# Kernel optimization log

Measured on AMD Instinct MI355X. Metric: run time of the kernel, lower is better.

Reference implementation:

```python
import jax, jax.numpy as jnp
import numpy as np
from jax import lax

B, P, ENC, DEC, ATT, EMB, V, L = 64, 196, 2048, 512, 512, 512, 10000, 30


def setup_inputs() -> dict:
    key = jax.random.key(0)
    ks = jax.random.split(key, 24)
    s = 0.02
    encoder_out = jax.random.normal(ks[0], (B, P, ENC), dtype=jnp.float32)
    encoded_captions = jax.random.randint(ks[1], (B, L), 0, V, dtype=jnp.int64)
    caption_lengths = jax.random.randint(ks[2], (B, 1), 2, L + 1, dtype=jnp.int64)
    # ensure max decode length == L-1 (matches torch max(decode_lengths))
    caption_lengths = caption_lengths.at[0, 0].set(L)
    p = lambda k, sh: jax.random.normal(k, sh, dtype=jnp.float32) * s
    return {
        "encoder_out": encoder_out,
        "encoded_captions": encoded_captions,
        "caption_lengths": caption_lengths,
        "W_enc": p(ks[3], (ATT, ENC)), "b_enc": jnp.zeros((ATT,), jnp.float32),
        "W_dec": p(ks[4], (ATT, DEC)), "b_dec": jnp.zeros((ATT,), jnp.float32),
        "w_full": p(ks[5], (ATT,)), "b_full": jnp.zeros((), jnp.float32),
        "emb_table": jax.random.uniform(ks[6], (V, EMB), jnp.float32, -0.1, 0.1),
        "W_ih": p(ks[7], (4 * DEC, EMB + ENC)), "b_ih": jnp.zeros((4 * DEC,), jnp.float32),
        "W_hh": p(ks[8], (4 * DEC, DEC)), "b_hh": jnp.zeros((4 * DEC,), jnp.float32),
        "W_init_h": p(ks[9], (DEC, ENC)), "b_init_h": jnp.zeros((DEC,), jnp.float32),
        "W_init_c": p(ks[10], (DEC, ENC)), "b_init_c": jnp.zeros((DEC,), jnp.float32),
        "W_beta": p(ks[11], (ENC, DEC)), "b_beta": jnp.zeros((ENC,), jnp.float32),
        "W_fc": jax.random.uniform(ks[12], (V, DEC), jnp.float32, -0.1, 0.1),
        "b_fc": jnp.zeros((V,), jnp.float32),
    }


def reference(encoder_out, encoded_captions, caption_lengths,
              W_enc, b_enc, W_dec, b_dec, w_full, b_full, emb_table,
              W_ih, b_ih, W_hh, b_hh, W_init_h, b_init_h, W_init_c, b_init_c,
              W_beta, b_beta, W_fc, b_fc):
    lengths = caption_lengths[:, 0]
    sort_ind = jnp.argsort(-lengths)  # descending, stable
    enc = encoder_out[sort_ind]            # [B,P,ENC]
    caps = encoded_captions[sort_ind]      # [B,L]
    dec_lens = lengths[sort_ind] - 1       # [B]
    T = caps.shape[1] - 1

    embs = emb_table[caps]                 # [B,L,EMB]
    mean_enc = enc.mean(axis=1)
    h0 = mean_enc @ W_init_h.T + b_init_h
    c0 = mean_enc @ W_init_c.T + b_init_c
    # encoder attention projection is h-independent: compute once
    att1 = jnp.einsum('bpe,ae->bpa', enc, W_enc) + b_enc  # [B,P,ATT]

    def step(carry, xs):
        h, c = carry
        emb_t, mask_t = xs  # [B,EMB], [B] bool
        att2 = h @ W_dec.T + b_dec                              # [B,ATT]
        e = jax.nn.relu(att1 + att2[:, None, :]) @ w_full + b_full  # [B,P]
        alpha = jax.nn.softmax(e, axis=1)
        awe = jnp.einsum('bp,bpe->be', alpha, enc)              # [B,ENC]
        gate = jax.nn.sigmoid(h @ W_beta.T + b_beta)
        awe = gate * awe
        x = jnp.concatenate([emb_t, awe], axis=1)               # [B,EMB+ENC]
        gates = x @ W_ih.T + b_ih + h @ W_hh.T + b_hh           # [B,4D]
        i, f, g, o = jnp.split(gates, 4, axis=1)
        i, f, o = jax.nn.sigmoid(i), jax.nn.sigmoid(f), jax.nn.sigmoid(o)
        g = jnp.tanh(g)
        c_new = f * c + i * g
        h_new = o * jnp.tanh(c_new)
        preds = h_new @ W_fc.T + b_fc                           # [B,V]  (dropout: eval/identity)
        m = mask_t[:, None].astype(preds.dtype)
        return (h_new, c_new), (preds * m, alpha * m)

    mask = jnp.arange(T)[:, None] < dec_lens[None, :]           # [T,B]
    embs_t = jnp.swapaxes(embs[:, :T], 0, 1)                    # [T,B,EMB]
    _, (preds, alphas) = lax.scan(step, (h0, c0), (embs_t, mask))
    predictions = jnp.swapaxes(preds, 0, 1)                     # [B,T,V]
    alphas = jnp.swapaxes(alphas, 0, 1)                         # [B,T,P]
    return predictions, alphas, caps, dec_lens, sort_ind
```

## Files before the change

### kernel.cpp

```cpp
#include <hip/hip_runtime.h>
#include <hip/hip_bf16.h>
#include <math.h>
#include <float.h>

#define BDIM   64
#define PDIM   196
#define ENC    2048
#define DECD   512
#define ATTD   512
#define EMBD   512
#define VOC    10000
#define LCAP   30
#define TSTEPS 29

typedef __attribute__((ext_vector_type(8))) short s8v;
typedef __attribute__((ext_vector_type(4))) float f4v;

__device__ __forceinline__ float sigf(float x) { return 1.0f / (1.0f + expf(-x)); }
__device__ __forceinline__ float bf2f(ushort u) { return __uint_as_float(((uint)u) << 16); }

__global__ void sort_kernel(const int* __restrict__ cap_len,
                            const int* __restrict__ caps,
                            int* __restrict__ sort_ind,
                            int* __restrict__ dec_lens,
                            int* __restrict__ caps_s,
                            float* __restrict__ out_caps,
                            float* __restrict__ out_dlen,
                            float* __restrict__ out_sind) {
    int i = threadIdx.x;
    __shared__ int len[BDIM];
    len[i] = cap_len[i];
    __syncthreads();
    int li = len[i];
    int r = 0;
    for (int j = 0; j < BDIM; ++j) {
        int lj = len[j];
        if (lj > li || (lj == li && j < i)) ++r;
    }
    sort_ind[r] = i;
    dec_lens[r] = li - 1;
    out_sind[r] = (float)i;
    out_dlen[r] = (float)(li - 1);
    for (int tt = 0; tt < LCAP; ++tt) {
        int v = caps[i * LCAP + tt];
        caps_s[r * LCAP + tt] = v;
        out_caps[r * LCAP + tt] = (float)v;
    }
}

__global__ __launch_bounds__(256) void conv_enc_kernel(const float* __restrict__ enc,
                                                       const int* __restrict__ sort_ind,
                                                       __hip_bfloat16* __restrict__ enc_s,
                                                       float* __restrict__ mean_enc) {
    int b = blockIdx.y, tid = threadIdx.x;
    int e = (blockIdx.x << 8) + tid;
    const float* ep = enc + (size_t)sort_ind[b] * (PDIM * ENC) + e;
    __hip_bfloat16* op = enc_s + (size_t)b * (PDIM * ENC) + e;
    float s = 0.f;
    for (int p = 0; p < PDIM; ++p) {
        float v = ep[(size_t)p * ENC];
        s += v;
        op[(size_t)p * ENC] = __float2bfloat16(v);
    }
    mean_enc[(size_t)b * ENC + e] = s * (1.0f / (float)PDIM);
}

__global__ __launch_bounds__(256) void f2b_kernel(const float* __restrict__ src,
                                                  __hip_bfloat16* __restrict__ dst, int n) {
    int i = blockIdx.x * 256 + threadIdx.x;
    if (i < n) dst[i] = __float2bfloat16(src[i]);
}

__global__ __launch_bounds__(256) void h0_kernel(const float* __restrict__ h0f,
                                                 __hip_bfloat16* __restrict__ xh) {
    int idx = blockIdx.x * 256 + threadIdx.x;
    int b = idx >> 9, j = idx & 511;
    xh[(size_t)b * 3072 + 2560 + j] = __float2bfloat16(h0f[idx]);
}

__global__ __launch_bounds__(256) void gemm32_k(
    const float* __restrict__ A, int lda,
    const float* __restrict__ W0, const float* __restrict__ bias0,
    float* __restrict__ C, int ldc, int K) {
    __shared__ float As[16][64];
    __shared__ float Ws[16][64];
    const int tid = threadIdx.x;
    const int tx = tid & 15, ty = tid >> 4;
    const int bn0 = blockIdx.x * 64;
    const int lr = tid >> 2;
    const int lk = (tid & 3) << 2;
    const float* Arow = A + (size_t)lr * lda;
    const int wn = bn0 + lr;
    float acc[4][4];
#pragma unroll
    for (int i = 0; i < 4; ++i)
#pragma unroll
        for (int j = 0; j < 4; ++j) acc[i][j] = 0.f;
    for (int k0 = 0; k0 < K; k0 += 16) {
        float4 av = *(const float4*)(Arow + k0 + lk);
        float4 wv = *(const float4*)(W0 + (size_t)wn * K + k0 + lk);
        __syncthreads();
        As[lk + 0][lr] = av.x; As[lk + 1][lr] = av.y;
        As[lk + 2][lr] = av.z; As[lk + 3][lr] = av.w;
        Ws[lk + 0][lr] = wv.x; Ws[lk + 1][lr] = wv.y;
        Ws[lk + 2][lr] = wv.z; Ws[lk + 3][lr] = wv.w;
        __syncthreads();
#pragma unroll
        for (int kk = 0; kk < 16; ++kk) {
            const float4 a = *(const float4*)&As[kk][ty << 2];
            const float4 w = *(const float4*)&Ws[kk][tx << 2];
            acc[0][0] += a.x * w.x; acc[0][1] += a.x * w.y; acc[0][2] += a.x * w.z; acc[0][3] += a.x * w.w;
            acc[1][0] += a.y * w.x; acc[1][1] += a.y * w.y; acc[1][2] += a.y * w.z; acc[1][3] += a.y * w.w;
            acc[2][0] += a.z * w.x; acc[2][1] += a.z * w.y; acc[2][2] += a.z * w.z; acc[2][3] += a.z * w.w;
            acc[3][0] += a.w * w.x; acc[3][1] += a.w * w.y; acc[3][2] += a.w * w.z; acc[3][3] += a.w * w.w;
        }
    }
#pragma unroll
    for (int i = 0; i < 4; ++i) {
        int row = (ty << 2) + i;
#pragma unroll
        for (int j = 0; j < 4; ++j) {
            int col = bn0 + (tx << 2) + j;
            C[(size_t)row * ldc + col] = acc[i][j] + bias0[col];
        }
    }
}

enum { E_ATT1 = 0, E_GACT = 1, E_GATES = 2, E_PREDS = 3 };

template <int MF, int MODE, int KA, int KB, bool XM>
__global__ __launch_bounds__(64) void mfma_gemm(
    const __hip_bfloat16* __restrict__ A, int lda,
    const __hip_bfloat16* __restrict__ W0, const __hip_bfloat16* __restrict__ W1,
    const float* __restrict__ bias0, const float* __restrict__ bias1,
    void* __restrict__ Cv,
    const int* __restrict__ dec_lens, int t) {
    const int l = threadIdx.x;
    const int c16 = l & 15, kg = l >> 4;
    const int n0 = (XM ? (int)blockIdx.y : (int)blockIdx.x) * 64;
    const int m0 = (XM ? (int)blockIdx.x : (int)blockIdx.y) * (16 * MF);

    f4v acc[MF][4];
#pragma unroll
    for (int mi = 0; mi < MF; ++mi)
#pragma unroll
        for (int ni = 0; ni < 4; ++ni) acc[mi][ni] = (f4v)0.0f;

    const __hip_bfloat16* arow[MF];
#pragma unroll
    for (int mi = 0; mi < MF; ++mi)
        arow[mi] = A + (size_t)(m0 + mi * 16 + c16) * lda + kg * 8;

    const __hip_bfloat16* w0r[4];
    const __hip_bfloat16* w1r[4];
#pragma unroll
    for (int ni = 0; ni < 4; ++ni) {
        int n = n0 + ni * 16 + c16;
        if (MODE == E_GACT) {
            w0r[ni] = (n < 2048) ? W0 + (size_t)n * 512 : W1 + (size_t)(n - 2048) * 512;
        } else if (MODE == E_GATES) {
            w0r[ni] = W0 + (size_t)n * (KA);
            w1r[ni] = W1 + (size_t)n * (KB);
        } else if (MODE == E_PREDS) {
            int nn = (n < VOC) ? n : (VOC - 1);
            w0r[ni] = W0 + (size_t)nn * KA;
        } else {
            w0r[ni] = W0 + (size_t)n * KA;
        }
        w0r[ni] += kg * 8;
        if (MODE == E_GATES) w1r[ni] += kg * 8;
    }

#pragma unroll 8
    for (int k0 = 0; k0 < KA; k0 += 32) {
        s8v a[MF], b[4];
#pragma unroll
        for (int mi = 0; mi < MF; ++mi) a[mi] = *(const s8v*)(arow[mi] + k0);
#pragma unroll
        for (int ni = 0; ni < 4; ++ni) b[ni] = *(const s8v*)(w0r[ni] + k0);
#pragma unroll
        for (int mi = 0; mi < MF; ++mi)
#pragma unroll
            for (int ni = 0; ni < 4; ++ni)
                acc[mi][ni] = __builtin_amdgcn_mfma_f32_16x16x32_bf16(a[mi], b[ni], acc[mi][ni], 0, 0, 0);
    }
    if constexpr (KB > 0) {
#pragma unroll
        for (int k0 = 0; k0 < KB; k0 += 32) {
            s8v a[MF], b[4];
#pragma unroll
            for (int mi = 0; mi < MF; ++mi) a[mi] = *(const s8v*)(arow[mi] + KA + k0);
#pragma unroll
            for (int ni = 0; ni < 4; ++ni) b[ni] = *(const s8v*)(w1r[ni] + k0);
#pragma unroll
            for (int mi = 0; mi < MF; ++mi)
#pragma unroll
                for (int ni = 0; ni < 4; ++ni)
                    acc[mi][ni] = __builtin_amdgcn_mfma_f32_16x16x32_bf16(a[mi], b[ni], acc[mi][ni], 0, 0, 0);
        }
    }

#pragma unroll
    for (int mi = 0; mi < MF; ++mi) {
#pragma unroll
        for (int ni = 0; ni < 4; ++ni) {
#pragma unroll
            for (int i = 0; i < 4; ++i) {
                int r = m0 + mi * 16 + kg * 4 + i;
                int c = n0 + ni * 16 + c16;
                float v = acc[mi][ni][i];
                if (MODE == E_ATT1) {
                    ((__hip_bfloat16*)Cv)[(size_t)r * 512 + c] = __float2bfloat16(v + bias0[c]);
                } else if (MODE == E_GACT) {
                    float* C = (float*)Cv;
                    if (c < 2048) C[(size_t)r * 2560 + c] = sigf(v + bias0[c]);
                    else          C[(size_t)r * 2560 + c] = v + bias1[c - 2048];
                } else if (MODE == E_GATES) {
                    ((float*)Cv)[(size_t)r * 2048 + c] = v + bias0[c] + bias1[c];
                } else {
                    if (c < VOC) {
                        float o = v + bias0[c];
                        ((float*)Cv)[(size_t)r * (TSTEPS * VOC) + (size_t)t * VOC + c] =
                            (t < dec_lens[r]) ? o : 0.f;
                    }
                }
            }
        }
    }
}

__global__ __launch_bounds__(256) void attawe_kernel(
    const __hip_bfloat16* __restrict__ att1, const float* __restrict__ gact,
    const __hip_bfloat16* __restrict__ enc_s,
    const float* __restrict__ w_full, const float* __restrict__ b_full,
    const float* __restrict__ emb_table,
    const int* __restrict__ caps_s, const int* __restrict__ dec_lens,
    __hip_bfloat16* __restrict__ xh, float* __restrict__ out_alphas, int t) {
    int b = blockIdx.x;
    int tid = threadIdx.x;
    __shared__ float s_att2[ATTD];
    __shared__ float s_wf[ATTD];
    __shared__ float s_e[PDIM];
    __shared__ float red[256];

    s_att2[tid]       = gact[(size_t)b * 2560 + 2048 + tid];
    s_att2[tid + 256] = gact[(size_t)b * 2560 + 2048 + 256 + tid];
    s_wf[tid]       = w_full[tid];
    s_wf[tid + 256] = w_full[tid + 256];
    __syncthreads();

    int wv = tid >> 6, lane = tid & 63;
    const float bf = b_full[0];
    const int a0 = lane << 3;
    for (int p = wv; p < PDIM; p += 4) {
        const ushort* row = (const ushort*)att1 + ((size_t)b * PDIM + p) * ATTD + a0;
        float s = 0.f;
#pragma unroll
        for (int i = 0; i < 8; ++i) {
            float x = bf2f(row[i]) + s_att2[a0 + i];
            s += fmaxf(x, 0.f) * s_wf[a0 + i];
        }
#pragma unroll
        for (int off = 32; off; off >>= 1) s += __shfl_xor(s, off);
        if (lane == 0) s_e[p] = s + bf;
    }
    __syncthreads();

    float v = (tid < PDIM) ? s_e[tid] : -FLT_MAX;
    red[tid] = v;
    __syncthreads();
    for (int st = 128; st; st >>= 1) {
        if (tid < st) red[tid] = fmaxf(red[tid], red[tid + st]);
        __syncthreads();
    }
    float mx = red[0];
    __syncthreads();
    float ex = (tid < PDIM) ? expf(v - mx) : 0.f;
    red[tid] = ex;
    __syncthreads();
    for (int st = 128; st; st >>= 1) {
        if (tid < st) red[tid] += red[tid + st];
        __syncthreads();
    }
    float inv = 1.f / red[0];
    __syncthreads();
    if (tid < PDIM) {
        float al = ex * inv;
        s_e[tid] = al;
        out_alphas[(size_t)b * (TSTEPS * PDIM) + (size_t)t * PDIM + tid] =
            (t < dec_lens[b]) ? al : 0.f;
    }
    __syncthreads();

    int e = tid << 3;
    const ushort* ep = (const ushort*)enc_s + (size_t)b * (PDIM * ENC) + e;
    float acc[8];
#pragma unroll
    for (int i = 0; i < 8; ++i) acc[i] = 0.f;
#pragma unroll 2
    for (int p = 0; p < PDIM; ++p) {
        float al = s_e[p];
        s8v u = *(const s8v*)(ep + (size_t)p * ENC);
#pragma unroll
        for (int i = 0; i < 8; ++i) acc[i] += al * bf2f((ushort)u[i]);
    }
    float4 g0 = *(const float4*)(gact + (size_t)b * 2560 + e);
    float4 g1 = *(const float4*)(gact + (size_t)b * 2560 + e + 4);
    __hip_bfloat16 ob[8];
    ob[0] = __float2bfloat16(acc[0] * g0.x); ob[1] = __float2bfloat16(acc[1] * g0.y);
    ob[2] = __float2bfloat16(acc[2] * g0.z); ob[3] = __float2bfloat16(acc[3] * g0.w);
    ob[4] = __float2bfloat16(acc[4] * g1.x); ob[5] = __float2bfloat16(acc[5] * g1.y);
    ob[6] = __float2bfloat16(acc[6] * g1.z); ob[7] = __float2bfloat16(acc[7] * g1.w);
    *(uint4*)(xh + (size_t)b * 3072 + 512 + e) = *(uint4*)ob;

    if (tid < 128) {
        int cap = caps_s[b * LCAP + t];
        int j = tid << 2;
        float4 em = *(const float4*)(emb_table + (size_t)cap * EMBD + j);
        __hip_bfloat16 eb[4];
        eb[0] = __float2bfloat16(em.x); eb[1] = __float2bfloat16(em.y);
        eb[2] = __float2bfloat16(em.z); eb[3] = __float2bfloat16(em.w);
        *(uint2*)(xh + (size_t)b * 3072 + j) = *(uint2*)eb;
    }
}

__global__ __launch_bounds__(256) void cell_kernel(const float* __restrict__ gates,
                                                   float* __restrict__ c,
                                                   __hip_bfloat16* __restrict__ xh) {
    int idx = blockIdx.x * 256 + threadIdx.x;
    int b = idx >> 9, j = idx & 511;
    const float* g = gates + (size_t)b * 2048;
    float i_ = sigf(g[j]);
    float f_ = sigf(g[512 + j]);
    float g_ = tanhf(g[1024 + j]);
    float o_ = sigf(g[1536 + j]);
    float cn = f_ * c[idx] + i_ * g_;
    c[idx] = cn;
    xh[(size_t)b * 3072 + 2560 + j] = __float2bfloat16(o_ * tanhf(cn));
}

extern "C" void kernel_launch(void* const* d_in, const int* in_sizes, int n_in,
                              void* d_out, int out_size, void* d_ws, size_t ws_size,
                              hipStream_t stream) {
    const float* enc      = (const float*)d_in[0];
    const int*   caps     = (const int*)d_in[1];
    const int*   clen     = (const int*)d_in[2];
    const float* W_enc    = (const float*)d_in[3];
    const float* b_enc    = (const float*)d_in[4];
    const float* W_dec    = (const float*)d_in[5];
    const float* b_dec    = (const float*)d_in[6];
    const float* w_full   = (const float*)d_in[7];
    const float* b_full   = (const float*)d_in[8];
    const float* emb_tab  = (const float*)d_in[9];
    const float* W_ih     = (const float*)d_in[10];
    const float* b_ih     = (const float*)d_in[11];
    const float* W_hh     = (const float*)d_in[12];
    const float* b_hh     = (const float*)d_in[13];
    const float* W_init_h = (const float*)d_in[14];
    const float* b_init_h = (const float*)d_in[15];
    const float* W_init_c = (const float*)d_in[16];
    const float* b_init_c = (const float*)d_in[17];
    const float* W_beta   = (const float*)d_in[18];
    const float* b_beta   = (const float*)d_in[19];
    const float* W_fc     = (const float*)d_in[20];
    const float* b_fc     = (const float*)d_in[21];

    float* out_pred = (float*)d_out;
    float* out_alph = out_pred + (size_t)BDIM * TSTEPS * VOC;
    float* out_caps = out_alph + (size_t)BDIM * TSTEPS * PDIM;
    float* out_dlen = out_caps + BDIM * LCAP;
    float* out_sind = out_dlen + BDIM;

    char* p = (char*)d_ws;
    auto carve = [&](size_t bytes) { char* r = p; p += (bytes + 255) & ~(size_t)255; return r; };
    int* sort_ind = (int*)carve(64 * 4);
    int* dec_lens = (int*)carve(64 * 4);
    int* caps_s   = (int*)carve(64 * LCAP * 4);
    float* mean_e = (float*)carve((size_t)64 * ENC * 4);
    float* h0f    = (float*)carve((size_t)64 * 512 * 4);
    float* cbuf   = (float*)carve((size_t)64 * 512 * 4);
    float* gact   = (float*)carve((size_t)64 * 2560 * 4);
    float* gates  = (float*)carve((size_t)64 * 2048 * 4);
    __hip_bfloat16* xh     = (__hip_bfloat16*)carve((size_t)64 * 3072 * 2);
    __hip_bfloat16* enc_s  = (__hip_bfloat16*)carve((size_t)64 * PDIM * ENC * 2);
    __hip_bfloat16* att1   = (__hip_bfloat16*)carve((size_t)64 * PDIM * 512 * 2);
    __hip_bfloat16* Wb_enc = (__hip_bfloat16*)carve((size_t)512 * 2048 * 2);
    __hip_bfloat16* Wb_bet = (__hip_bfloat16*)carve((size_t)2048 * 512 * 2);
    __hip_bfloat16* Wb_dec = (__hip_bfloat16*)carve((size_t)512 * 512 * 2);
    __hip_bfloat16* Wb_ih  = (__hip_bfloat16*)carve((size_t)2048 * 2560 * 2);
    __hip_bfloat16* Wb_hh  = (__hip_bfloat16*)carve((size_t)2048 * 512 * 2);
    __hip_bfloat16* Wb_fc  = (__hip_bfloat16*)carve((size_t)VOC * 512 * 2);

    sort_kernel<<<1, 64, 0, stream>>>(clen, caps, sort_ind, dec_lens, caps_s,
                                      out_caps, out_dlen, out_sind);
    conv_enc_kernel<<<dim3(8, 64), 256, 0, stream>>>(enc, sort_ind, enc_s, mean_e);
    f2b_kernel<<<(512 * 2048 + 255) / 256, 256, 0, stream>>>(W_enc, Wb_enc, 512 * 2048);
    f2b_kernel<<<(2048 * 512 + 255) / 256, 256, 0, stream>>>(W_beta, Wb_bet, 2048 * 512);
    f2b_kernel<<<(512 * 512 + 255) / 256, 256, 0, stream>>>(W_dec, Wb_dec, 512 * 512);
    f2b_kernel<<<(2048 * 2560 + 255) / 256, 256, 0, stream>>>(W_ih, Wb_ih, 2048 * 2560);
    f2b_kernel<<<(2048 * 512 + 255) / 256, 256, 0, stream>>>(W_hh, Wb_hh, 2048 * 512);
    f2b_kernel<<<(VOC * 512 + 255) / 256, 256, 0, stream>>>(W_fc, Wb_fc, VOC * 512);

    gemm32_k<<<dim3(8, 1), 256, 0, stream>>>(mean_e, ENC, W_init_h, b_init_h, h0f, 512, ENC);
    gemm32_k<<<dim3(8, 1), 256, 0, stream>>>(mean_e, ENC, W_init_c, b_init_c, cbuf, 512, ENC);
    h0_kernel<<<128, 256, 0, stream>>>(h0f, xh);

    mfma_gemm<2, E_ATT1, 2048, 0, true><<<dim3(392, 8), 64, 0, stream>>>(
        enc_s, ENC, Wb_enc, nullptr, b_enc, nullptr, att1, nullptr, 0);

    for (int t = 0; t < TSTEPS; ++t) {
        mfma_gemm<1, E_GACT, 512, 0, false><<<dim3(40, 4), 64, 0, stream>>>(
            xh + 2560, 3072, Wb_bet, Wb_dec, b_beta, b_dec, gact, nullptr, 0);
        attawe_kernel<<<64, 256, 0, stream>>>(att1, gact, enc_s, w_full, b_full,
                                              emb_tab, caps_s, dec_lens, xh,
                                              out_alph, t);
        mfma_gemm<1, E_GATES, 2560, 512, false><<<dim3(32, 4), 64, 0, stream>>>(
            xh, 3072, Wb_ih, Wb_hh, b_ih, b_hh, gates, nullptr, 0);
        cell_kernel<<<128, 256, 0, stream>>>(gates, cbuf, xh);
        mfma_gemm<1, E_PREDS, 512, 0, false><<<dim3(160, 4), 64, 0, stream>>>(
            xh + 2560, 3072, Wb_fc, nullptr, b_fc, nullptr, out_pred, dec_lens, t);
    }
}
```

Measured before the change: 3.655 ms.

## Batch vocab projection after loop, split-K recurrent GEMMs, prefetch MFMA operands

The per-step vocabulary projection is taken out of the recurrence. Each step's hidden state is stored, and a single large GEMM over all 29×64 rows runs after the loop. The gate and attention-projection GEMMs are split along K into two partial buffers so more workgroups run in each step, and bias, sigmoid and sum are folded into the attawe and cell kernels. A three-slot register prefetch pipeline is added to the shared MFMA inner loop. This costs extra partial-sum traffic and an hstore buffer in exchange for shorter serial steps and better weight reuse in the FC projection.

```diff
diff --git a/kernel.cpp b/kernel.cpp
--- a/kernel.cpp
+++ b/kernel.cpp
@@ -18,6 +18,31 @@
 
 __device__ __forceinline__ float sigf(float x) { return 1.0f / (1.0f + expf(-x)); }
 __device__ __forceinline__ float bf2f(ushort u) { return __uint_as_float(((uint)u) << 16); }
+
+template <int MF, int NIT>
+__device__ __forceinline__ void gemm_seg(const __hip_bfloat16* const* arow,
+                                         const __hip_bfloat16* const* wrow,
+                                         f4v acc[][4]) {
+    s8v aP[3][MF], bP[3][4];
+    auto LD = [&](int it, int slot) {
+#pragma unroll
+        for (int mi = 0; mi < MF; ++mi) aP[slot][mi] = *(const s8v*)(arow[mi] + it * 32);
+#pragma unroll
+        for (int ni = 0; ni < 4; ++ni)  bP[slot][ni] = *(const s8v*)(wrow[ni] + it * 32);
+    };
+    LD(0, 0);
+    if constexpr (NIT > 1) LD(1, 1);
+#pragma unroll
+    for (int it = 0; it < NIT; ++it) {
+        if (it + 2 < NIT) LD(it + 2, (it + 2) % 3);
+        const int s = it % 3;
+#pragma unroll
+        for (int mi = 0; mi < MF; ++mi)
+#pragma unroll
+            for (int ni = 0; ni < 4; ++ni)
+                acc[mi][ni] = __builtin_amdgcn_mfma_f32_16x16x32_bf16(aP[s][mi], bP[s][ni], acc[mi][ni], 0, 0, 0);
+    }
+}
 
 __global__ void sort_kernel(const int* __restrict__ cap_len,
                             const int* __restrict__ caps,
@@ -126,116 +151,159 @@
     }
 }
 
-enum { E_ATT1 = 0, E_GACT = 1, E_GATES = 2, E_PREDS = 3 };
-
-template <int MF, int MODE, int KA, int KB, bool XM>
-__global__ __launch_bounds__(64) void mfma_gemm(
-    const __hip_bfloat16* __restrict__ A, int lda,
-    const __hip_bfloat16* __restrict__ W0, const __hip_bfloat16* __restrict__ W1,
-    const float* __restrict__ bias0, const float* __restrict__ bias1,
-    void* __restrict__ Cv,
-    const int* __restrict__ dec_lens, int t) {
-    const int l = threadIdx.x;
-    const int c16 = l & 15, kg = l >> 4;
-    const int n0 = (XM ? (int)blockIdx.y : (int)blockIdx.x) * 64;
-    const int m0 = (XM ? (int)blockIdx.x : (int)blockIdx.y) * (16 * MF);
-
-    f4v acc[MF][4];
-#pragma unroll
-    for (int mi = 0; mi < MF; ++mi)
+__global__ __launch_bounds__(64) void att1_gemm(
+    const __hip_bfloat16* __restrict__ A, const __hip_bfloat16* __restrict__ W,
+    const float* __restrict__ bias, __hip_bfloat16* __restrict__ C) {
+    const int l = threadIdx.x, c16 = l & 15, kg = l >> 4;
+    const int m0 = blockIdx.x * 32, n0 = blockIdx.y * 64;
+    f4v acc[2][4];
+#pragma unroll
+    for (int mi = 0; mi < 2; ++mi)
 #pragma unroll
         for (int ni = 0; ni < 4; ++ni) acc[mi][ni] = (f4v)0.0f;
-
-    const __hip_bfloat16* arow[MF];
-#pragma unroll
-    for (int mi = 0; mi < MF; ++mi)
-        arow[mi] = A + (size_t)(m0 + mi * 16 + c16) * lda + kg * 8;
-
-    const __hip_bfloat16* w0r[4];
-    const __hip_bfloat16* w1r[4];
-#pragma unroll
-    for (int ni = 0; ni < 4; ++ni) {
-        int n = n0 + ni * 16 + c16;
-        if (MODE == E_GACT) {
-            w0r[ni] = (n < 2048) ? W0 + (size_t)n * 512 : W1 + (size_t)(n - 2048) * 512;
-        } else if (MODE == E_GATES) {
-            w0r[ni] = W0 + (size_t)n * (KA);
-            w1r[ni] = W1 + (size_t)n * (KB);
-        } else if (MODE == E_PREDS) {
-            int nn = (n < VOC) ? n : (VOC - 1);
-            w0r[ni] = W0 + (size_t)nn * KA;
-        } else {
-            w0r[ni] = W0 + (size_t)n * KA;
-        }
-        w0r[ni] += kg * 8;
-        if (MODE == E_GATES) w1r[ni] += kg * 8;
-    }
-
-#pragma unroll 8
-    for (int k0 = 0; k0 < KA; k0 += 32) {
-        s8v a[MF], b[4];
-#pragma unroll
-        for (int mi = 0; mi < MF; ++mi) a[mi] = *(const s8v*)(arow[mi] + k0);
-#pragma unroll
-        for (int ni = 0; ni < 4; ++ni) b[ni] = *(const s8v*)(w0r[ni] + k0);
-#pragma unroll
-        for (int mi = 0; mi < MF; ++mi)
-#pragma unroll
-            for (int ni = 0; ni < 4; ++ni)
-                acc[mi][ni] = __builtin_amdgcn_mfma_f32_16x16x32_bf16(a[mi], b[ni], acc[mi][ni], 0, 0, 0);
-    }
-    if constexpr (KB > 0) {
-#pragma unroll
-        for (int k0 = 0; k0 < KB; k0 += 32) {
-            s8v a[MF], b[4];
-#pragma unroll
-            for (int mi = 0; mi < MF; ++mi) a[mi] = *(const s8v*)(arow[mi] + KA + k0);
-#pragma unroll
-            for (int ni = 0; ni < 4; ++ni) b[ni] = *(const s8v*)(w1r[ni] + k0);
-#pragma unroll
-            for (int mi = 0; mi < MF; ++mi)
-#pragma unroll
-                for (int ni = 0; ni < 4; ++ni)
-                    acc[mi][ni] = __builtin_amdgcn_mfma_f32_16x16x32_bf16(a[mi], b[ni], acc[mi][ni], 0, 0, 0);
-        }
-    }
-
-#pragma unroll
-    for (int mi = 0; mi < MF; ++mi) {
-#pragma unroll
-        for (int ni = 0; ni < 4; ++ni) {
+    const __hip_bfloat16* arow[2];
+#pragma unroll
+    for (int mi = 0; mi < 2; ++mi)
+        arow[mi] = A + (size_t)(m0 + mi * 16 + c16) * ENC + kg * 8;
+    const __hip_bfloat16* wrow[4];
+#pragma unroll
+    for (int ni = 0; ni < 4; ++ni)
+        wrow[ni] = W + (size_t)(n0 + ni * 16 + c16) * ENC + kg * 8;
+    gemm_seg<2, 64>(arow, wrow, acc);
+#pragma unroll
+    for (int mi = 0; mi < 2; ++mi)
+#pragma unroll
+        for (int ni = 0; ni < 4; ++ni)
 #pragma unroll
             for (int i = 0; i < 4; ++i) {
                 int r = m0 + mi * 16 + kg * 4 + i;
                 int c = n0 + ni * 16 + c16;
-                float v = acc[mi][ni][i];
-                if (MODE == E_ATT1) {
-                    ((__hip_bfloat16*)Cv)[(size_t)r * 512 + c] = __float2bfloat16(v + bias0[c]);
-                } else if (MODE == E_GACT) {
-                    float* C = (float*)Cv;
-                    if (c < 2048) C[(size_t)r * 2560 + c] = sigf(v + bias0[c]);
-                    else          C[(size_t)r * 2560 + c] = v + bias1[c - 2048];
-                } else if (MODE == E_GATES) {
-                    ((float*)Cv)[(size_t)r * 2048 + c] = v + bias0[c] + bias1[c];
-                } else {
-                    if (c < VOC) {
-                        float o = v + bias0[c];
-                        ((float*)Cv)[(size_t)r * (TSTEPS * VOC) + (size_t)t * VOC + c] =
-                            (t < dec_lens[r]) ? o : 0.f;
-                    }
+                C[(size_t)r * 512 + c] = __float2bfloat16(acc[mi][ni][i] + bias[c]);
+            }
+}
+
+__global__ __launch_bounds__(64) void gact_gemm(
+    const __hip_bfloat16* __restrict__ H,
+    const __hip_bfloat16* __restrict__ Wb,
+    const __hip_bfloat16* __restrict__ Wd,
+    float* __restrict__ P) {
+    const int l = threadIdx.x, c16 = l & 15, kg = l >> 4;
+    const int n0 = blockIdx.x * 64, m0 = blockIdx.y * 16, z = blockIdx.z;
+    const int ko = z * 256;
+    f4v acc[1][4];
+#pragma unroll
+    for (int ni = 0; ni < 4; ++ni) acc[0][ni] = (f4v)0.0f;
+    const __hip_bfloat16* arow[1] = { H + (size_t)(m0 + c16) * 3072 + ko + kg * 8 };
+    const __hip_bfloat16* wrow[4];
+#pragma unroll
+    for (int ni = 0; ni < 4; ++ni) {
+        int n = n0 + ni * 16 + c16;
+        wrow[ni] = ((n < 2048) ? Wb + (size_t)n * 512 : Wd + (size_t)(n - 2048) * 512) + ko + kg * 8;
+    }
+    gemm_seg<1, 8>(arow, wrow, acc);
+    float* Pz = P + (size_t)z * (64 * 2560);
+#pragma unroll
+    for (int ni = 0; ni < 4; ++ni)
+#pragma unroll
+        for (int i = 0; i < 4; ++i) {
+            int r = m0 + kg * 4 + i;
+            int c = n0 + ni * 16 + c16;
+            Pz[(size_t)r * 2560 + c] = acc[0][ni][i];
+        }
+}
+
+__global__ __launch_bounds__(64) void gates_gemm(
+    const __hip_bfloat16* __restrict__ X,
+    const __hip_bfloat16* __restrict__ Wih,
+    const __hip_bfloat16* __restrict__ Whh,
+    float* __restrict__ P) {
+    const int l = threadIdx.x, c16 = l & 15, kg = l >> 4;
+    const int n0 = blockIdx.x * 64, m0 = blockIdx.y * 16, z = blockIdx.z;
+    f4v acc[1][4];
+#pragma unroll
+    for (int ni = 0; ni < 4; ++ni) acc[0][ni] = (f4v)0.0f;
+    const __hip_bfloat16* arow[1];
+    const __hip_bfloat16* wrow[4];
+    if (z == 0) {
+        arow[0] = X + (size_t)(m0 + c16) * 3072 + kg * 8;
+#pragma unroll
+        for (int ni = 0; ni < 4; ++ni)
+            wrow[ni] = Wih + (size_t)(n0 + ni * 16 + c16) * 2560 + kg * 8;
+        gemm_seg<1, 48>(arow, wrow, acc);
+    } else {
+        arow[0] = X + (size_t)(m0 + c16) * 3072 + 1536 + kg * 8;
+#pragma unroll
+        for (int ni = 0; ni < 4; ++ni)
+            wrow[ni] = Wih + (size_t)(n0 + ni * 16 + c16) * 2560 + 1536 + kg * 8;
+        gemm_seg<1, 32>(arow, wrow, acc);
+        arow[0] = X + (size_t)(m0 + c16) * 3072 + 2560 + kg * 8;
+#pragma unroll
+        for (int ni = 0; ni < 4; ++ni)
+            wrow[ni] = Whh + (size_t)(n0 + ni * 16 + c16) * 512 + kg * 8;
+        gemm_seg<1, 16>(arow, wrow, acc);
+    }
+    float* Pz = P + (size_t)z * (64 * 2048);
+#pragma unroll
+    for (int ni = 0; ni < 4; ++ni)
+#pragma unroll
+        for (int i = 0; i < 4; ++i) {
+            int r = m0 + kg * 4 + i;
+            int c = n0 + ni * 16 + c16;
+            Pz[(size_t)r * 2048 + c] = acc[0][ni][i];
+        }
+}
+
+__global__ __launch_bounds__(64) void predsb_gemm(
+    const __hip_bfloat16* __restrict__ Hs,
+    const __hip_bfloat16* __restrict__ Wfc,
+    const float* __restrict__ bias,
+    const int* __restrict__ dec_lens,
+    float* __restrict__ out) {
+    const int l = threadIdx.x, c16 = l & 15, kg = l >> 4;
+    const int n0 = blockIdx.x * 64, m0 = blockIdx.y * 32;
+    f4v acc[2][4];
+#pragma unroll
+    for (int mi = 0; mi < 2; ++mi)
+#pragma unroll
+        for (int ni = 0; ni < 4; ++ni) acc[mi][ni] = (f4v)0.0f;
+    const __hip_bfloat16* arow[2];
+#pragma unroll
+    for (int mi = 0; mi < 2; ++mi)
+        arow[mi] = Hs + (size_t)(m0 + mi * 16 + c16) * 512 + kg * 8;
+    const __hip_bfloat16* wrow[4];
+#pragma unroll
+    for (int ni = 0; ni < 4; ++ni) {
+        int n = n0 + ni * 16 + c16;
+        int nn = (n < VOC) ? n : (VOC - 1);
+        wrow[ni] = Wfc + (size_t)nn * 512 + kg * 8;
+    }
+    gemm_seg<2, 16>(arow, wrow, acc);
+#pragma unroll
+    for (int mi = 0; mi < 2; ++mi)
+#pragma unroll
+        for (int ni = 0; ni < 4; ++ni)
+#pragma unroll
+            for (int i = 0; i < 4; ++i) {
+                int r = m0 + mi * 16 + kg * 4 + i;
+                int c = n0 + ni * 16 + c16;
+                if (c < VOC) {
+                    int tt = r >> 6, b = r & 63;
+                    float v = acc[mi][ni][i] + bias[c];
+                    out[(size_t)b * (TSTEPS * VOC) + (size_t)tt * VOC + c] =
+                        (tt < dec_lens[b]) ? v : 0.f;
                 }
             }
-        }
-    }
 }
 
 __global__ __launch_bounds__(256) void attawe_kernel(
-    const __hip_bfloat16* __restrict__ att1, const float* __restrict__ gact,
+    const __hip_bfloat16* __restrict__ att1, const float* __restrict__ gactp,
     const __hip_bfloat16* __restrict__ enc_s,
     const float* __restrict__ w_full, const float* __restrict__ b_full,
+    const float* __restrict__ b_dec, const float* __restrict__ b_beta,
     const float* __restrict__ emb_table,
     const int* __restrict__ caps_s, const int* __restrict__ dec_lens,
     __hip_bfloat16* __restrict__ xh, float* __restrict__ out_alphas, int t) {
+    const int G = 64 * 2560;
     int b = blockIdx.x;
     int tid = threadIdx.x;
     __shared__ float s_att2[ATTD];
@@ -243,8 +311,9 @@
     __shared__ float s_e[PDIM];
     __shared__ float red[256];
 
-    s_att2[tid]       = gact[(size_t)b * 2560 + 2048 + tid];
-    s_att2[tid + 256] = gact[(size_t)b * 2560 + 2048 + 256 + tid];
+    const float* gb = gactp + (size_t)b * 2560;
+    s_att2[tid]       = gb[2048 + tid]       + gb[G + 2048 + tid]       + b_dec[tid];
+    s_att2[tid + 256] = gb[2048 + 256 + tid] + gb[G + 2048 + 256 + tid] + b_dec[256 + tid];
     s_wf[tid]       = w_full[tid];
     s_wf[tid + 256] = w_full[tid + 256];
     __syncthreads();
@@ -304,13 +373,20 @@
 #pragma unroll
         for (int i = 0; i < 8; ++i) acc[i] += al * bf2f((ushort)u[i]);
     }
-    float4 g0 = *(const float4*)(gact + (size_t)b * 2560 + e);
-    float4 g1 = *(const float4*)(gact + (size_t)b * 2560 + e + 4);
+    float4 p00 = *(const float4*)(gb + e);
+    float4 p01 = *(const float4*)(gb + e + 4);
+    float4 p10 = *(const float4*)(gb + G + e);
+    float4 p11 = *(const float4*)(gb + G + e + 4);
+    float4 bb0 = *(const float4*)(b_beta + e);
+    float4 bb1 = *(const float4*)(b_beta + e + 4);
+    float g[8];
+    g[0] = sigf(p00.x + p10.x + bb0.x); g[1] = sigf(p00.y + p10.y + bb0.y);
+    g[2] = sigf(p00.z + p10.z + bb0.z); g[3] = sigf(p00.w + p10.w + bb0.w);
+    g[4] = sigf(p01.x + p11.x + bb1.x); g[5] = sigf(p01.y + p11.y + bb1.y);
+    g[6] = sigf(p01.z + p11.z + bb1.z); g[7] = sigf(p01.w + p11.w + bb1.w);
     __hip_bfloat16 ob[8];
-    ob[0] = __float2bfloat16(acc[0] * g0.x); ob[1] = __float2bfloat16(acc[1] * g0.y);
-    ob[2] = __float2bfloat16(acc[2] * g0.z); ob[3] = __float2bfloat16(acc[3] * g0.w);
-    ob[4] = __float2bfloat16(acc[4] * g1.x); ob[5] = __float2bfloat16(acc[5] * g1.y);
-    ob[6] = __float2bfloat16(acc[6] * g1.z); ob[7] = __float2bfloat16(acc[7] * g1.w);
+#pragma unroll
+    for (int i = 0; i < 8; ++i) ob[i] = __float2bfloat16(acc[i] * g[i]);
     *(uint4*)(xh + (size_t)b * 3072 + 512 + e) = *(uint4*)ob;
 
     if (tid < 128) {
@@ -324,19 +400,25 @@
     }
 }
 
-__global__ __launch_bounds__(256) void cell_kernel(const float* __restrict__ gates,
-                                                   float* __restrict__ c,
-                                                   __hip_bfloat16* __restrict__ xh) {
+__global__ __launch_bounds__(256) void cell_kernel(
+    const float* __restrict__ gatesp, const float* __restrict__ b_ih,
+    const float* __restrict__ b_hh, float* __restrict__ c,
+    __hip_bfloat16* __restrict__ xh, __hip_bfloat16* __restrict__ hstore, int t) {
+    const int GS = 64 * 2048;
     int idx = blockIdx.x * 256 + threadIdx.x;
     int b = idx >> 9, j = idx & 511;
-    const float* g = gates + (size_t)b * 2048;
-    float i_ = sigf(g[j]);
-    float f_ = sigf(g[512 + j]);
-    float g_ = tanhf(g[1024 + j]);
-    float o_ = sigf(g[1536 + j]);
-    float cn = f_ * c[idx] + i_ * g_;
+    const float* g0 = gatesp + (size_t)b * 2048;
+    const float* g1 = gatesp + GS + (size_t)b * 2048;
+    float vi = g0[j]        + g1[j]        + b_ih[j]        + b_hh[j];
+    float vf = g0[512 + j]  + g1[512 + j]  + b_ih[512 + j]  + b_hh[512 + j];
+    float vg = g0[1024 + j] + g1[1024 + j] + b_ih[1024 + j] + b_hh[1024 + j];
+    float vo = g0[1536 + j] + g1[1536 + j] + b_ih[1536 + j] + b_hh[1536 + j];
+    float i_ = sigf(vi), f_ = sigf(vf), gg = tanhf(vg), o_ = sigf(vo);
+    float cn = f_ * c[idx] + i_ * gg;
     c[idx] = cn;
-    xh[(size_t)b * 3072 + 2560 + j] = __float2bfloat16(o_ * tanhf(cn));
+    __hip_bfloat16 hb = __float2bfloat16(o_ * tanhf(cn));
+    xh[(size_t)b * 3072 + 2560 + j] = hb;
+    hstore[(size_t)t * (64 * 512) + idx] = hb;
 }
 
 extern "C" void kernel_launch(void* const* d_in, const int* in_sizes, int n_in,
@@ -379,9 +461,10 @@
     float* mean_e = (float*)carve((size_t)64 * ENC * 4);
     float* h0f    = (float*)carve((size_t)64 * 512 * 4);
     float* cbuf   = (float*)carve((size_t)64 * 512 * 4);
-    float* gact   = (float*)carve((size_t)64 * 2560 * 4);
-    float* gates  = (float*)carve((size_t)64 * 2048 * 4);
+    float* gactp  = (float*)carve((size_t)2 * 64 * 2560 * 4);
+    float* gatesp = (float*)carve((size_t)2 * 64 * 2048 * 4);
     __hip_bfloat16* xh     = (__hip_bfloat16*)carve((size_t)64 * 3072 * 2);
+    __hip_bfloat16* hstore = (__hip_bfloat16*)carve((size_t)TSTEPS * 64 * 512 * 2);
     __hip_bfloat16* enc_s  = (__hip_bfloat16*)carve((size_t)64 * PDIM * ENC * 2);
     __hip_bfloat16* att1   = (__hip_bfloat16*)carve((size_t)64 * PDIM * 512 * 2);
     __hip_bfloat16* Wb_enc = (__hip_bfloat16*)carve((size_t)512 * 2048 * 2);
@@ -405,19 +488,16 @@
     gemm32_k<<<dim3(8, 1), 256, 0, stream>>>(mean_e, ENC, W_init_c, b_init_c, cbuf, 512, ENC);
     h0_kernel<<<128, 256, 0, stream>>>(h0f, xh);
 
-    mfma_gemm<2, E_ATT1, 2048, 0, true><<<dim3(392, 8), 64, 0, stream>>>(
-        enc_s, ENC, Wb_enc, nullptr, b_enc, nullptr, att1, nullptr, 0);
+    att1_gemm<<<dim3(392, 8), 64, 0, stream>>>(enc_s, Wb_enc, b_enc, att1);
 
     for (int t = 0; t < TSTEPS; ++t) {
-        mfma_gemm<1, E_GACT, 512, 0, false><<<dim3(40, 4), 64, 0, stream>>>(
-            xh + 2560, 3072, Wb_bet, Wb_dec, b_beta, b_dec, gact, nullptr, 0);
-        attawe_kernel<<<64, 256, 0, stream>>>(att1, gact, enc_s, w_full, b_full,
-                                              emb_tab, caps_s, dec_lens, xh,
-                                              out_alph, t);
-        mfma_gemm<1, E_GATES, 2560, 512, false><<<dim3(32, 4), 64, 0, stream>>>(
-            xh, 3072, Wb_ih, Wb_hh, b_ih, b_hh, gates, nullptr, 0);
-        cell_kernel<<<128, 256, 0, stream>>>(gates, cbuf, xh);
-        mfma_gemm<1, E_PREDS, 512, 0, false><<<dim3(160, 4), 64, 0, stream>>>(
-            xh + 2560, 3072, Wb_fc, nullptr, b_fc, nullptr, out_pred, dec_lens, t);
-    }
-}
+        gact_gemm<<<dim3(40, 4, 2), 64, 0, stream>>>(xh + 2560, Wb_bet, Wb_dec, gactp);
+        attawe_kernel<<<64, 256, 0, stream>>>(att1, gactp, enc_s, w_full, b_full,
+                                              b_dec, b_beta, emb_tab, caps_s,
+                                              dec_lens, xh, out_alph, t);
+        gates_gemm<<<dim3(32, 4, 2), 64, 0, stream>>>(xh, Wb_ih, Wb_hh, gatesp);
+        cell_kernel<<<128, 256, 0, stream>>>(gatesp, b_ih, b_hh, cbuf, xh, hstore, t);
+    }
+
+    predsb_gemm<<<dim3(160, 58), 64, 0, stream>>>(hstore, Wb_fc, b_fc, dec_lens, out_pred);
+}
```

After: 3.251 ms. 11.0% less time.
